# Optimization experiments

Hardware: AMD Instinct MI355X
Metric: run time of the kernel (lower is better)

The kernel has to match this reference:

```python
import jax, jax.numpy as jnp
import numpy as np
import math

DIM = 2048
NUM_HEADS = 16
NUM_KV_HEADS = 4
HEAD_DIM = DIM // NUM_HEADS  # 128
KV_DIM = DIM * NUM_KV_HEADS // NUM_HEADS  # 512
B, T = 4, 2048


def setup_inputs() -> dict:
    key = jax.random.key(0)
    ks = jax.random.split(key, 12)
    s = 0.02
    return {
        "x": jax.random.normal(ks[0], (B, T, DIM), dtype=jnp.float32),
        "cos": jax.random.uniform(ks[1], (T, HEAD_DIM // 2), dtype=jnp.float32),
        "sin": jax.random.uniform(ks[2], (T, HEAD_DIM // 2), dtype=jnp.float32),
        "Wq": jax.random.normal(ks[3], (DIM, DIM), dtype=jnp.float32) * s,
        "bq": jnp.zeros((DIM,), dtype=jnp.float32),
        "Wk": jax.random.normal(ks[4], (DIM, KV_DIM), dtype=jnp.float32) * s,
        "bk": jnp.zeros((KV_DIM,), dtype=jnp.float32),
        "Wv": jax.random.normal(ks[5], (DIM, KV_DIM), dtype=jnp.float32) * s,
        "bv": jnp.zeros((KV_DIM,), dtype=jnp.float32),
        "Wo": jax.random.normal(ks[6], (DIM, DIM), dtype=jnp.float32) * s,
        "bo": jnp.zeros((DIM,), dtype=jnp.float32),
    }


def _rope(t, cos, sin):
    # t: [B, H, T, D]; cos/sin: [T, D/2] broadcast over (B, H)
    t1, t2 = t[..., ::2], t[..., 1::2]
    return jnp.concatenate([t1 * cos - t2 * sin, t1 * sin + t2 * cos], axis=-1)


def reference(x, cos, sin, Wq, bq, Wk, bk, Wv, bv, Wo, bo):
    Bx, Tx, C = x.shape
    q = (x @ Wq + bq).reshape(Bx, Tx, NUM_HEADS, HEAD_DIM).transpose(0, 2, 1, 3)
    k = (x @ Wk + bk).reshape(Bx, Tx, NUM_KV_HEADS, HEAD_DIM).transpose(0, 2, 1, 3)
    v = (x @ Wv + bv).reshape(Bx, Tx, NUM_KV_HEADS, HEAD_DIM).transpose(0, 2, 1, 3)
    rep = NUM_HEADS // NUM_KV_HEADS
    k = jnp.repeat(k, rep, axis=1)
    v = jnp.repeat(v, rep, axis=1)
    q = _rope(q, cos, sin)
    k = _rope(k, cos, sin)
    scores = jnp.einsum("bhqd,bhkd->bhqk", q, k) / math.sqrt(HEAD_DIM)
    attn = jax.nn.softmax(scores, axis=-1)
    out = jnp.einsum("bhqk,bhkd->bhqd", attn, v)
    out = out.transpose(0, 2, 1, 3).reshape(Bx, Tx, C)
    return out @ Wo + bo
```

## Files before the change

### kernel.cpp

```cpp
#include <hip/hip_runtime.h>

typedef unsigned short u16;
using bf16x8 = __attribute__((ext_vector_type(8))) short;
using u16x8  = __attribute__((ext_vector_type(8))) unsigned short;
using f32x4  = __attribute__((ext_vector_type(4))) float;
using u32x2  = __attribute__((ext_vector_type(2))) unsigned int;

__device__ __forceinline__ u16 f2bf(float f) {
  unsigned u = __float_as_uint(f);
  u += 0x7FFFu + ((u >> 16) & 1u);
  return (u16)(u >> 16);
}

__device__ __forceinline__ unsigned cvt_pk_bf16(float lo, float hi) {
  unsigned r;
  asm("v_cvt_pk_bf16_f32 %0, %1, %2" : "=v"(r) : "v"(lo), "v"(hi));
  return r;
}

__device__ __forceinline__ void gload_lds16(const void* g, void* l) {
  __builtin_amdgcn_global_load_lds(
      (const __attribute__((address_space(1))) unsigned int*)g,
      (__attribute__((address_space(3))) unsigned int*)l, 16, 0, 0);
}

__global__ __launch_bounds__(256) void k_cvt(const float* __restrict__ src,
                                             u16* __restrict__ dst) {
  size_t i = (size_t)blockIdx.x * 256 + threadIdx.x;
  const float4* s4 = (const float4*)src;
  float4 a = s4[i * 2], b = s4[i * 2 + 1];
  u16x8 r;
  r[0] = f2bf(a.x); r[1] = f2bf(a.y); r[2] = f2bf(a.z); r[3] = f2bf(a.w);
  r[4] = f2bf(b.x); r[5] = f2bf(b.y); r[6] = f2bf(b.z); r[7] = f2bf(b.w);
  *(u16x8*)(dst + i * 8) = r;
}

__global__ void k_transpose_cvt(const float* __restrict__ src, u16* __restrict__ dst,
                                int R, int C) {
  __shared__ float tile[32][33];
  int bx = blockIdx.x * 32, by = blockIdx.y * 32;
  int tx = threadIdx.x, ty = threadIdx.y;
#pragma unroll
  for (int j = 0; j < 4; ++j)
    tile[ty + j * 8][tx] = src[(size_t)(by + ty + j * 8) * C + bx + tx];
  __syncthreads();
#pragma unroll
  for (int j = 0; j < 4; ++j)
    dst[(size_t)(bx + ty + j * 8) * R + by + tx] = f2bf(tile[tx][ty + j * 8]);
}

__device__ __forceinline__ void gemm_core128(const u16* __restrict__ A,
                                             const u16* __restrict__ Bt, int K,
                                             int m0, int n0, u16* As, u16* Bs,
                                             f32x4 acc[4][4]) {
  const int tid  = threadIdx.x;
  const int lane = tid & 63;
  const int w    = tid >> 6;
  const int wr   = (w >> 1) * 64;
  const int wc   = (w & 1) * 64;
  const int srow = (w << 3) + (lane >> 3);
  const int scol = (lane & 7) << 3;
  const int lm   = lane & 15;
  const int lk   = (lane >> 4) << 3;

  for (int kt = 0; kt < K; kt += 64) {
#pragma unroll
    for (int i = 0; i < 4; ++i) {
      int r = (i << 5) + srow;
      gload_lds16(A  + (size_t)(m0 + r) * K + kt + scol, As + ((i * 4 + w) << 9));
      gload_lds16(Bt + (size_t)(n0 + r) * K + kt + scol, Bs + ((i * 4 + w) << 9));
    }
    __syncthreads();
#pragma unroll
    for (int kk = 0; kk < 64; kk += 32) {
      bf16x8 af[4], bfr[4];
#pragma unroll
      for (int m = 0; m < 4; ++m)
        af[m] = *(const bf16x8*)(As + (wr + m * 16 + lm) * 64 + kk + lk);
#pragma unroll
      for (int n = 0; n < 4; ++n)
        bfr[n] = *(const bf16x8*)(Bs + (wc + n * 16 + lm) * 64 + kk + lk);
#pragma unroll
      for (int m = 0; m < 4; ++m)
#pragma unroll
        for (int n = 0; n < 4; ++n)
          acc[m][n] = __builtin_amdgcn_mfma_f32_16x16x32_bf16(af[m], bfr[n], acc[m][n], 0, 0, 0);
    }
    __syncthreads();
  }
}

__global__ __launch_bounds__(256, 2) void k_qkv(
    const u16* __restrict__ xb, const u16* __restrict__ wT,
    const float* __restrict__ bq, const float* __restrict__ bk, const float* __restrict__ bv,
    const float* __restrict__ cosb, const float* __restrict__ sinb,
    u16* __restrict__ qbuf, u16* __restrict__ kbuf, u16* __restrict__ vbufT) {
  __shared__ u16 As[128 * 64], Bs[128 * 64];
  const int mt = blockIdx.x, nt = blockIdx.y;
  f32x4 acc[4][4];
#pragma unroll
  for (int m = 0; m < 4; ++m)
#pragma unroll
    for (int n = 0; n < 4; ++n) { f32x4 z = {0.f, 0.f, 0.f, 0.f}; acc[m][n] = z; }
  gemm_core128(xb, wT, 2048, mt * 128, nt * 128, As, Bs, acc);

  const int lane = threadIdx.x & 63, w = threadIdx.x >> 6;
  const int row0 = mt * 128 + (w >> 1) * 64 + ((lane >> 4) << 2);
  const int col0 = nt * 128 + (w & 1) * 64 + (lane & 15);
  const float qscale = 0.12751744f;

#pragma unroll
  for (int m = 0; m < 4; ++m) {
#pragma unroll
    for (int n = 0; n < 4; ++n) {
      const int gc = col0 + n * 16;
#pragma unroll
      for (int i = 0; i < 4; ++i) {
        const int gr = row0 + m * 16 + i;
        const int b = gr >> 11, t = gr & 2047;
        float v = acc[m][n][i];
        if (nt < 16) {
          int h = gc >> 7, d = gc & 127;
          float val = v + bq[gc];
          float part = __shfl_xor(val, 1);
          int ir = d >> 1;
          float c = cosb[t * 64 + ir], s = sinb[t * 64 + ir];
          float outv; int dd;
          if (d & 1) { outv = part * s + val * c; dd = ir + 64; }
          else       { outv = val * c - part * s; dd = ir; }
          qbuf[(((size_t)(b * 16 + h) * 2048 + t) << 7) + dd] = f2bf(outv * qscale);
        } else if (nt < 20) {
          int g2 = gc - 2048;
          int kvh = g2 >> 7, d = g2 & 127;
          float val = v + bk[g2];
          float part = __shfl_xor(val, 1);
          int ir = d >> 1;
          float c = cosb[t * 64 + ir], s = sinb[t * 64 + ir];
          float outv; int dd;
          if (d & 1) { outv = part * s + val * c; dd = ir + 64; }
          else       { outv = val * c - part * s; dd = ir; }
          kbuf[(((size_t)(b * 4 + kvh) * 2048 + t) << 7) + dd] = f2bf(outv);
        } else {
          int g2 = gc - 2560;
          int kvh = g2 >> 7, d = g2 & 127;
          float val = v + bv[g2];
          vbufT[((size_t)((b * 4 + kvh) * 128 + d)) * 2048 + t] = f2bf(val);
        }
      }
    }
  }
}

__global__ __launch_bounds__(256, 2) void k_attn(const u16* __restrict__ qbuf,
                                                 const u16* __restrict__ kbuf,
                                                 const u16* __restrict__ vbufT,
                                                 u16* __restrict__ ob) {
  __shared__ u16 Ks[2][64 * 128];
  __shared__ u16 Vs[2][128 * 64];
  __shared__ u16 Ps[128 * 64];

  const int f = blockIdx.x;
  const int x = f & 7, mm = f >> 3;
  const int g = x * 2 + (mm >> 6);
  const int mem = mm & 63;
  const int b = g >> 2, kvh = g & 3;
  const int h = kvh * 4 + (mem >> 4);
  const int qt = mem & 15;

  const int tid = threadIdx.x, lane = tid & 63, w = tid >> 6;
  const int lm = lane & 15, lg = lane >> 4;

  const u16* qb = qbuf + ((size_t)((b * 16 + h) * 2048 + qt * 128)) * 128;
  const u16* kb = kbuf + ((size_t)(b * 4 + kvh) * 2048) * 128;
  const u16* vb = vbufT + ((size_t)(b * 4 + kvh) * 128) * 2048;

  bf16x8 qf[2][4];
#pragma unroll
  for (int st = 0; st < 2; ++st)
#pragma unroll
    for (int dc = 0; dc < 4; ++dc)
      qf[st][dc] = *(const bf16x8*)(qb + (size_t)(w * 32 + st * 16 + lm) * 128 + dc * 32 + (lg << 3));

  f32x4 o[2][8];
#pragma unroll
  for (int st = 0; st < 2; ++st)
#pragma unroll
    for (int dn = 0; dn < 8; ++dn) { f32x4 z = {0.f, 0.f, 0.f, 0.f}; o[st][dn] = z; }
  float lsum[2] = {0.f, 0.f};

  auto stage = [&](int buf, int kt) {
#pragma unroll
    for (int j = 0; j < 4; ++j) {
      int s  = w * 4 + j;
      int cK = s * 64 + lane;
      int rK = cK >> 4, ccK = cK & 15;
      gload_lds16(kb + (size_t)(kt + rK) * 128 + ((ccK ^ (rK & 7)) << 3), &Ks[buf][s << 9]);
      int dV = s * 8 + (lane >> 3), ccV = lane & 7;
      gload_lds16(vb + (size_t)dV * 2048 + kt + ((ccV ^ (dV & 7)) << 3), &Vs[buf][s << 9]);
    }
  };

  stage(0, 0);
  int cur = 0;
  for (int t = 0; t < 32; ++t) {
    const int kt = t << 6;
    if (t < 31) {
      stage(cur ^ 1, kt + 64);
      asm volatile("s_waitcnt vmcnt(8)" ::: "memory");
    } else {
      asm volatile("s_waitcnt vmcnt(0)" ::: "memory");
    }
    __builtin_amdgcn_s_barrier();
    __builtin_amdgcn_sched_barrier(0);
    const u16* KsC = Ks[cur];
    const u16* VsC = Vs[cur];

#pragma unroll
    for (int kg = 0; kg < 4; ++kg) {
      const int krow = kg * 16 + lm;
      bf16x8 kf[4];
#pragma unroll
      for (int dc = 0; dc < 4; ++dc)
        kf[dc] = *(const bf16x8*)(KsC + krow * 128 + (((dc * 4 + lg) ^ (krow & 7)) << 3));
      f32x4 s0 = {0.f, 0.f, 0.f, 0.f}, s1 = {0.f, 0.f, 0.f, 0.f};
      __builtin_amdgcn_s_setprio(1);
#pragma unroll
      for (int dc = 0; dc < 4; ++dc) {
        s0 = __builtin_amdgcn_mfma_f32_16x16x32_bf16(kf[dc], qf[0][dc], s0, 0, 0, 0);
        s1 = __builtin_amdgcn_mfma_f32_16x16x32_bf16(kf[dc], qf[1][dc], s1, 0, 0, 0);
      }
      __builtin_amdgcn_s_setprio(0);
#pragma unroll
      for (int st = 0; st < 2; ++st) {
        f32x4 sv = st ? s1 : s0;
        float p0 = __builtin_amdgcn_exp2f(sv[0]);
        float p1 = __builtin_amdgcn_exp2f(sv[1]);
        float p2 = __builtin_amdgcn_exp2f(sv[2]);
        float p3 = __builtin_amdgcn_exp2f(sv[3]);
        lsum[st] += (p0 + p1) + (p2 + p3);
        u32x2 pk;
        pk[0] = cvt_pk_bf16(p0, p1);
        pk[1] = cvt_pk_bf16(p2, p3);
        const int q = w * 32 + st * 16 + lm;
        const int chunk = kg * 2 + (lg >> 1);
        u16* dst = Ps + q * 64 + ((chunk ^ (q & 7)) << 3) + ((lg & 1) << 2);
        *reinterpret_cast<u32x2*>(dst) = pk;
      }
    }

#pragma unroll
    for (int kstep = 0; kstep < 2; ++kstep) {
      bf16x8 pf[2];
#pragma unroll
      for (int st = 0; st < 2; ++st) {
        const int q = w * 32 + st * 16 + lm;
        pf[st] = *(const bf16x8*)(Ps + q * 64 + (((kstep * 4 + lg) ^ (q & 7)) << 3));
      }
      __builtin_amdgcn_s_setprio(1);
#pragma unroll
      for (int dn = 0; dn < 8; ++dn) {
        const int d = dn * 16 + lm;
        bf16x8 vf = *(const bf16x8*)(VsC + d * 64 + (((kstep * 4 + lg) ^ (d & 7)) << 3));
        o[0][dn] = __builtin_amdgcn_mfma_f32_16x16x32_bf16(pf[0], vf, o[0][dn], 0, 0, 0);
        o[1][dn] = __builtin_amdgcn_mfma_f32_16x16x32_bf16(pf[1], vf, o[1][dn], 0, 0, 0);
      }
      __builtin_amdgcn_s_setprio(0);
    }
    __builtin_amdgcn_sched_barrier(0);
    __builtin_amdgcn_s_barrier();
    cur ^= 1;
  }

#pragma unroll
  for (int st = 0; st < 2; ++st) {
    float L = lsum[st];
    L += __shfl_xor(L, 16);
    L += __shfl_xor(L, 32);
#pragma unroll
    for (int i = 0; i < 4; ++i) {
      float inv = 1.0f / __shfl(L, lg * 4 + i);
      int t = qt * 128 + w * 32 + st * 16 + lg * 4 + i;
#pragma unroll
      for (int dn = 0; dn < 8; ++dn) {
        int d = dn * 16 + lm;
        ob[((size_t)(b * 2048 + t)) * 2048 + h * 128 + d] = f2bf(o[st][dn][i] * inv);
      }
    }
  }
}

__global__ __launch_bounds__(256, 2) void k_oproj(const u16* __restrict__ ab,
                                                  const u16* __restrict__ woT,
                                                  const float* __restrict__ bo,
                                                  float* __restrict__ out) {
  __shared__ u16 As[128 * 64], Bs[128 * 64];
  const int mt = blockIdx.x, nt = blockIdx.y;
  f32x4 acc[4][4];
#pragma unroll
  for (int m = 0; m < 4; ++m)
#pragma unroll
    for (int n = 0; n < 4; ++n) { f32x4 z = {0.f, 0.f, 0.f, 0.f}; acc[m][n] = z; }
  gemm_core128(ab, woT, 2048, mt * 128, nt * 128, As, Bs, acc);

  const int lane = threadIdx.x & 63, w = threadIdx.x >> 6;
  const int row0 = mt * 128 + (w >> 1) * 64 + ((lane >> 4) << 2);
  const int col0 = nt * 128 + (w & 1) * 64 + (lane & 15);
#pragma unroll
  for (int m = 0; m < 4; ++m)
#pragma unroll
    for (int n = 0; n < 4; ++n) {
      const int gc = col0 + n * 16;
      const float bias = bo[gc];
#pragma unroll
      for (int i = 0; i < 4; ++i) {
        const int gr = row0 + m * 16 + i;
        out[(size_t)gr * 2048 + gc] = acc[m][n][i] + bias;
      }
    }
}

extern "C" void kernel_launch(void* const* d_in, const int* in_sizes, int n_in,
                              void* d_out, int out_size, void* d_ws, size_t ws_size,
                              hipStream_t stream) {
  const float* x    = (const float*)d_in[0];
  const float* cosb = (const float*)d_in[1];
  const float* sinb = (const float*)d_in[2];
  const float* Wq   = (const float*)d_in[3];
  const float* bq   = (const float*)d_in[4];
  const float* Wk   = (const float*)d_in[5];
  const float* bk   = (const float*)d_in[6];
  const float* Wv   = (const float*)d_in[7];
  const float* bv   = (const float*)d_in[8];
  const float* Wo   = (const float*)d_in[9];
  const float* bo   = (const float*)d_in[10];
  float* out = (float*)d_out;

  u16* ws    = (u16*)d_ws;
  u16* xb    = ws;
  u16* wqkvT = xb    + (size_t)8192 * 2048;
  u16* woT   = wqkvT + (size_t)3072 * 2048;
  u16* qbuf  = woT   + (size_t)2048 * 2048;
  u16* kbuf  = qbuf  + (size_t)8192 * 2048;
  u16* vbufT = kbuf  + (size_t)8192 * 512;
  u16* attn  = xb;

  k_cvt<<<8192, 256, 0, stream>>>(x, xb);
  dim3 tb(32, 8);
  k_transpose_cvt<<<dim3(64, 64), tb, 0, stream>>>(Wq, wqkvT, 2048, 2048);
  k_transpose_cvt<<<dim3(16, 64), tb, 0, stream>>>(Wk, wqkvT + (size_t)2048 * 2048, 2048, 512);
  k_transpose_cvt<<<dim3(16, 64), tb, 0, stream>>>(Wv, wqkvT + (size_t)2560 * 2048, 2048, 512);
  k_transpose_cvt<<<dim3(64, 64), tb, 0, stream>>>(Wo, woT, 2048, 2048);

  k_qkv<<<dim3(64, 24), 256, 0, stream>>>(xb, wqkvT, bq, bk, bv, cosb, sinb, qbuf, kbuf, vbufT);
  k_attn<<<1024, 256, 0, stream>>>(qbuf, kbuf, vbufT, attn);
  k_oproj<<<dim3(64, 16), 256, 0, stream>>>(attn, woT, bo, out);
}
```

Before: 404.4 us.

## Replace 128x128 GEMMs with double-buffered swizzled 256x256 templated GEMM kernel

New measurement: 444.1 us. 1.1x slower.

```diff
diff --git a/kernel.cpp b/kernel.cpp
--- a/kernel.cpp
+++ b/kernel.cpp
@@ -49,102 +49,143 @@
     dst[(size_t)(bx + ty + j * 8) * R + by + tx] = f2bf(tile[tx][ty + j * 8]);
 }
 
-__device__ __forceinline__ void gemm_core128(const u16* __restrict__ A,
-                                             const u16* __restrict__ Bt, int K,
-                                             int m0, int n0, u16* As, u16* Bs,
-                                             f32x4 acc[4][4]) {
-  const int tid  = threadIdx.x;
-  const int lane = tid & 63;
-  const int w    = tid >> 6;
-  const int wr   = (w >> 1) * 64;
-  const int wc   = (w & 1) * 64;
-  const int srow = (w << 3) + (lane >> 3);
-  const int scol = (lane & 7) << 3;
-  const int lm   = lane & 15;
-  const int lk   = (lane >> 4) << 3;
-
-  for (int kt = 0; kt < K; kt += 64) {
-#pragma unroll
-    for (int i = 0; i < 4; ++i) {
-      int r = (i << 5) + srow;
-      gload_lds16(A  + (size_t)(m0 + r) * K + kt + scol, As + ((i * 4 + w) << 9));
-      gload_lds16(Bt + (size_t)(n0 + r) * K + kt + scol, Bs + ((i * 4 + w) << 9));
-    }
-    __syncthreads();
-#pragma unroll
-    for (int kk = 0; kk < 64; kk += 32) {
-      bf16x8 af[4], bfr[4];
-#pragma unroll
-      for (int m = 0; m < 4; ++m)
-        af[m] = *(const bf16x8*)(As + (wr + m * 16 + lm) * 64 + kk + lk);
-#pragma unroll
-      for (int n = 0; n < 4; ++n)
-        bfr[n] = *(const bf16x8*)(Bs + (wc + n * 16 + lm) * 64 + kk + lk);
-#pragma unroll
-      for (int m = 0; m < 4; ++m)
-#pragma unroll
-        for (int n = 0; n < 4; ++n)
-          acc[m][n] = __builtin_amdgcn_mfma_f32_16x16x32_bf16(af[m], bfr[n], acc[m][n], 0, 0, 0);
-    }
-    __syncthreads();
-  }
-}
-
-__global__ __launch_bounds__(256, 2) void k_qkv(
-    const u16* __restrict__ xb, const u16* __restrict__ wT,
+template <int EPI>
+__global__ __launch_bounds__(512, 2) void k_gemm256(
+    const u16* __restrict__ A, const u16* __restrict__ Bt,
     const float* __restrict__ bq, const float* __restrict__ bk, const float* __restrict__ bv,
     const float* __restrict__ cosb, const float* __restrict__ sinb,
-    u16* __restrict__ qbuf, u16* __restrict__ kbuf, u16* __restrict__ vbufT) {
-  __shared__ u16 As[128 * 64], Bs[128 * 64];
-  const int mt = blockIdx.x, nt = blockIdx.y;
-  f32x4 acc[4][4];
-#pragma unroll
-  for (int m = 0; m < 4; ++m)
-#pragma unroll
-    for (int n = 0; n < 4; ++n) { f32x4 z = {0.f, 0.f, 0.f, 0.f}; acc[m][n] = z; }
-  gemm_core128(xb, wT, 2048, mt * 128, nt * 128, As, Bs, acc);
-
-  const int lane = threadIdx.x & 63, w = threadIdx.x >> 6;
-  const int row0 = mt * 128 + (w >> 1) * 64 + ((lane >> 4) << 2);
-  const int col0 = nt * 128 + (w & 1) * 64 + (lane & 15);
+    u16* __restrict__ qbuf, u16* __restrict__ kbuf, u16* __restrict__ vbufT,
+    const float* __restrict__ bo, float* __restrict__ fout, int ntiles) {
+  __shared__ u16 As[2][2][128 * 64];
+  __shared__ u16 Bs[2][2][128 * 64];
+
+  const int nwg = 32 * ntiles;
+  const int per = nwg >> 3;
+  const int sid = ((int)blockIdx.x & 7) * per + ((int)blockIdx.x >> 3);
+  const int mt = sid & 31;
+  const int nt = sid >> 5;
+
+  const int tid = threadIdx.x, lane = tid & 63, w = tid >> 6;
+  const int lm = lane & 15, lg = lane >> 4;
+  const int wr = w >> 2, wc = w & 3;
+
+  const u16* Abase = A  + (size_t)mt * 256 * 2048;
+  const u16* Bbase = Bt + (size_t)nt * 256 * 2048;
+
+  f32x4 acc[8][4];
+#pragma unroll
+  for (int mf = 0; mf < 8; ++mf)
+#pragma unroll
+    for (int nf = 0; nf < 4; ++nf) { f32x4 z = {0.f, 0.f, 0.f, 0.f}; acc[mf][nf] = z; }
+
+  auto stage = [&](int d, int kt) {
+#pragma unroll
+    for (int j = 0; j < 2; ++j) {
+      const int s = w * 2 + j;
+      const int c = s * 64 + lane;
+      const int row = c >> 3;
+      const int col = ((c & 7) ^ (row & 7)) << 3;
+#pragma unroll
+      for (int h = 0; h < 2; ++h) {
+        gload_lds16(Abase + (size_t)(h * 128 + row) * 2048 + kt + col, &As[d][h][s * 512]);
+        gload_lds16(Bbase + (size_t)(h * 128 + row) * 2048 + kt + col, &Bs[d][h][s * 512]);
+      }
+    }
+  };
+
+  stage(0, 0);
+  for (int t = 0; t < 32; ++t) {
+    if (t < 31) {
+      stage((t + 1) & 1, (t + 1) << 6);
+      asm volatile("s_waitcnt vmcnt(8)" ::: "memory");
+    } else {
+      asm volatile("s_waitcnt vmcnt(0)" ::: "memory");
+    }
+    __builtin_amdgcn_s_barrier();
+    __builtin_amdgcn_sched_barrier(0);
+
+    const int d = t & 1;
+    const u16* Ah = &As[d][wr][0];
+    const u16* Bh = &Bs[d][wc >> 1][0];
+    const int brow0 = (wc & 1) * 64;
+
+    bf16x8 bfr[4][2];
+#pragma unroll
+    for (int nf = 0; nf < 4; ++nf)
+#pragma unroll
+      for (int k2 = 0; k2 < 2; ++k2) {
+        const int row = brow0 + nf * 16 + lm;
+        bfr[nf][k2] = *(const bf16x8*)(Bh + row * 64 + ((((k2 << 2) + lg) ^ (lm & 7)) << 3));
+      }
+#pragma unroll
+    for (int mp = 0; mp < 4; ++mp) {
+      bf16x8 af[2][2];
+#pragma unroll
+      for (int mi = 0; mi < 2; ++mi)
+#pragma unroll
+        for (int k2 = 0; k2 < 2; ++k2) {
+          const int row = (mp * 2 + mi) * 16 + lm;
+          af[mi][k2] = *(const bf16x8*)(Ah + row * 64 + ((((k2 << 2) + lg) ^ (lm & 7)) << 3));
+        }
+      __builtin_amdgcn_s_setprio(1);
+#pragma unroll
+      for (int mi = 0; mi < 2; ++mi)
+#pragma unroll
+        for (int k2 = 0; k2 < 2; ++k2)
+#pragma unroll
+          for (int nf = 0; nf < 4; ++nf)
+            acc[mp * 2 + mi][nf] = __builtin_amdgcn_mfma_f32_16x16x32_bf16(
+                af[mi][k2], bfr[nf][k2], acc[mp * 2 + mi][nf], 0, 0, 0);
+      __builtin_amdgcn_s_setprio(0);
+    }
+    __builtin_amdgcn_sched_barrier(0);
+    __builtin_amdgcn_s_barrier();
+  }
+
+  const int row0 = mt * 256 + wr * 128 + lg * 4;
+  const int col0 = nt * 256 + wc * 64 + lm;
   const float qscale = 0.12751744f;
 
 #pragma unroll
-  for (int m = 0; m < 4; ++m) {
-#pragma unroll
-    for (int n = 0; n < 4; ++n) {
-      const int gc = col0 + n * 16;
+  for (int mf = 0; mf < 8; ++mf) {
+#pragma unroll
+    for (int nf = 0; nf < 4; ++nf) {
+      const int gc = col0 + nf * 16;
 #pragma unroll
       for (int i = 0; i < 4; ++i) {
-        const int gr = row0 + m * 16 + i;
-        const int b = gr >> 11, t = gr & 2047;
-        float v = acc[m][n][i];
-        if (nt < 16) {
-          int h = gc >> 7, d = gc & 127;
-          float val = v + bq[gc];
-          float part = __shfl_xor(val, 1);
-          int ir = d >> 1;
-          float c = cosb[t * 64 + ir], s = sinb[t * 64 + ir];
-          float outv; int dd;
-          if (d & 1) { outv = part * s + val * c; dd = ir + 64; }
-          else       { outv = val * c - part * s; dd = ir; }
-          qbuf[(((size_t)(b * 16 + h) * 2048 + t) << 7) + dd] = f2bf(outv * qscale);
-        } else if (nt < 20) {
-          int g2 = gc - 2048;
-          int kvh = g2 >> 7, d = g2 & 127;
-          float val = v + bk[g2];
-          float part = __shfl_xor(val, 1);
-          int ir = d >> 1;
-          float c = cosb[t * 64 + ir], s = sinb[t * 64 + ir];
-          float outv; int dd;
-          if (d & 1) { outv = part * s + val * c; dd = ir + 64; }
-          else       { outv = val * c - part * s; dd = ir; }
-          kbuf[(((size_t)(b * 4 + kvh) * 2048 + t) << 7) + dd] = f2bf(outv);
+        const int gr = row0 + mf * 16 + i;
+        float v = acc[mf][nf][i];
+        if (EPI == 1) {
+          fout[(size_t)gr * 2048 + gc] = v + bo[gc];
         } else {
-          int g2 = gc - 2560;
-          int kvh = g2 >> 7, d = g2 & 127;
-          float val = v + bv[g2];
-          vbufT[((size_t)((b * 4 + kvh) * 128 + d)) * 2048 + t] = f2bf(val);
+          const int b = gr >> 11, tt = gr & 2047;
+          if (nt < 8) {
+            const int h = gc >> 7, dd0 = gc & 127;
+            float val = v + bq[gc];
+            float part = __shfl_xor(val, 1);
+            const int ir = dd0 >> 1;
+            float c = cosb[tt * 64 + ir], s = sinb[tt * 64 + ir];
+            float outv; int dd;
+            if (dd0 & 1) { outv = part * s + val * c; dd = ir + 64; }
+            else         { outv = val * c - part * s; dd = ir; }
+            qbuf[(((size_t)(b * 16 + h) * 2048 + tt) << 7) + dd] = f2bf(outv * qscale);
+          } else if (nt < 10) {
+            const int g2 = gc - 2048;
+            const int kvh = g2 >> 7, dd0 = g2 & 127;
+            float val = v + bk[g2];
+            float part = __shfl_xor(val, 1);
+            const int ir = dd0 >> 1;
+            float c = cosb[tt * 64 + ir], s = sinb[tt * 64 + ir];
+            float outv; int dd;
+            if (dd0 & 1) { outv = part * s + val * c; dd = ir + 64; }
+            else         { outv = val * c - part * s; dd = ir; }
+            kbuf[(((size_t)(b * 4 + kvh) * 2048 + tt) << 7) + dd] = f2bf(outv);
+          } else {
+            const int g2 = gc - 2560;
+            const int kvh = g2 >> 7, dd0 = g2 & 127;
+            float val = v + bv[g2];
+            vbufT[((size_t)((b * 4 + kvh) * 128 + dd0)) * 2048 + tt] = f2bf(val);
+          }
         }
       }
     }
@@ -287,36 +328,6 @@
       }
     }
   }
-}
-
-__global__ __launch_bounds__(256, 2) void k_oproj(const u16* __restrict__ ab,
-                                                  const u16* __restrict__ woT,
-                                                  const float* __restrict__ bo,
-                                                  float* __restrict__ out) {
-  __shared__ u16 As[128 * 64], Bs[128 * 64];
-  const int mt = blockIdx.x, nt = blockIdx.y;
-  f32x4 acc[4][4];
-#pragma unroll
-  for (int m = 0; m < 4; ++m)
-#pragma unroll
-    for (int n = 0; n < 4; ++n) { f32x4 z = {0.f, 0.f, 0.f, 0.f}; acc[m][n] = z; }
-  gemm_core128(ab, woT, 2048, mt * 128, nt * 128, As, Bs, acc);
-
-  const int lane = threadIdx.x & 63, w = threadIdx.x >> 6;
-  const int row0 = mt * 128 + (w >> 1) * 64 + ((lane >> 4) << 2);
-  const int col0 = nt * 128 + (w & 1) * 64 + (lane & 15);
-#pragma unroll
-  for (int m = 0; m < 4; ++m)
-#pragma unroll
-    for (int n = 0; n < 4; ++n) {
-      const int gc = col0 + n * 16;
-      const float bias = bo[gc];
-#pragma unroll
-      for (int i = 0; i < 4; ++i) {
-        const int gr = row0 + m * 16 + i;
-        out[(size_t)gr * 2048 + gc] = acc[m][n][i] + bias;
-      }
-    }
 }
 
 extern "C" void kernel_launch(void* const* d_in, const int* in_sizes, int n_in,
@@ -351,7 +362,9 @@
   k_transpose_cvt<<<dim3(16, 64), tb, 0, stream>>>(Wv, wqkvT + (size_t)2560 * 2048, 2048, 512);
   k_transpose_cvt<<<dim3(64, 64), tb, 0, stream>>>(Wo, woT, 2048, 2048);
 
-  k_qkv<<<dim3(64, 24), 256, 0, stream>>>(xb, wqkvT, bq, bk, bv, cosb, sinb, qbuf, kbuf, vbufT);
+  k_gemm256<0><<<384, 512, 0, stream>>>(xb, wqkvT, bq, bk, bv, cosb, sinb,
+                                        qbuf, kbuf, vbufT, nullptr, nullptr, 12);
   k_attn<<<1024, 256, 0, stream>>>(qbuf, kbuf, vbufT, attn);
-  k_oproj<<<dim3(64, 16), 256, 0, stream>>>(attn, woT, bo, out);
-}
+  k_gemm256<1><<<256, 512, 0, stream>>>(attn, woT, nullptr, nullptr, nullptr, nullptr, nullptr,
+                                        nullptr, nullptr, nullptr, bo, out, 8);
+}
```
